# Kernel optimization log

Hardware: AMD Instinct MI355X
Metric: run time of the kernel (lower is better)

## Reference

```python
import jax, jax.numpy as jnp
import numpy as np
import math

D_MODEL, D_K, N_HEADS = 1024, 64, 16
N, T = 2, 2048


def setup_inputs() -> dict:
    key = jax.random.key(0)
    ks = jax.random.split(key, 12)
    s = 1.0 / math.sqrt(D_MODEL)
    dh = D_K * N_HEADS
    return {
        "k": jax.random.normal(ks[0], (N, T, D_MODEL), jnp.float32),
        "q": jax.random.normal(ks[1], (N, T, D_MODEL), jnp.float32),
        "v": jax.random.normal(ks[2], (N, T, D_MODEL), jnp.float32),
        "mask": jnp.ones((N, T), jnp.int32),
        "Wk": jax.random.normal(ks[3], (D_MODEL, dh), jnp.float32) * s,
        "bk": jnp.zeros((dh,), jnp.float32),
        "Wq": jax.random.normal(ks[4], (D_MODEL, dh), jnp.float32) * s,
        "bq": jnp.zeros((dh,), jnp.float32),
        "Wv": jax.random.normal(ks[5], (D_MODEL, dh), jnp.float32) * s,
        "bv": jnp.zeros((dh,), jnp.float32),
        "Wo": jax.random.normal(ks[6], (dh, D_MODEL), jnp.float32) * (1.0 / math.sqrt(dh)),
        "bo": jnp.zeros((D_MODEL,), jnp.float32),
    }


def reference(k, q, v, mask, Wk, bk, Wq, bq, Wv, bv, Wo, bo):
    n, t = k.shape[0], k.shape[1]
    # project and split heads -> (N, H, T, d_k)
    K = (k @ Wk + bk).reshape(n, t, N_HEADS, D_K).transpose(0, 2, 1, 3)
    Q = (q @ Wq + bq).reshape(n, t, N_HEADS, D_K).transpose(0, 2, 1, 3)
    V = (v @ Wv + bv).reshape(n, t, N_HEADS, D_K).transpose(0, 2, 1, 3)
    scores = jnp.einsum("bhqd,bhkd->bhqk", Q, K) / math.sqrt(D_K)
    scores = jnp.where(mask[:, None, None, :] == 0, -jnp.inf, scores)
    weights = jax.nn.softmax(scores, axis=-1)
    A = jnp.einsum("bhqk,bhkd->bhqd", weights, V)
    A = A.transpose(0, 2, 1, 3).reshape(n, t, N_HEADS * D_K)
    return A @ Wo + bo
```

## Files before the change

kernel.cpp:

```cpp
#include <hip/hip_runtime.h>


typedef __bf16 bf16;
typedef __bf16 bf16x8 __attribute__((ext_vector_type(8)));
typedef __bf16 bf16x4 __attribute__((ext_vector_type(4)));
typedef float f32x4 __attribute__((ext_vector_type(4)));

#define MFMA16(a, b, c) __builtin_amdgcn_mfma_f32_16x16x32_bf16((a), (b), (c), 0, 0, 0)

__device__ __forceinline__ void load_lds16(const bf16* g, bf16* l) {
  __builtin_amdgcn_global_load_lds(
      (const __attribute__((address_space(1))) unsigned int*)g,
      (__attribute__((address_space(3))) unsigned int*)l, 16, 0, 0);
}

__device__ __forceinline__ bf16x8 cvt8(const float* __restrict__ p) {
  const f32x4 a = *(const f32x4*)p;
  const f32x4 b = *(const f32x4*)(p + 4);
  bf16x8 r;
  r[0] = (bf16)a[0]; r[1] = (bf16)a[1]; r[2] = (bf16)a[2]; r[3] = (bf16)a[3];
  r[4] = (bf16)b[0]; r[5] = (bf16)b[1]; r[6] = (bf16)b[2]; r[7] = (bf16)b[3];
  return r;
}

__global__ __launch_bounds__(256) void convert3(const float* __restrict__ a,
                                                const float* __restrict__ b,
                                                const float* __restrict__ c,
                                                bf16* __restrict__ oa,
                                                bf16* __restrict__ ob,
                                                bf16* __restrict__ oc) {
  const size_t i = ((size_t)blockIdx.x * 256 + threadIdx.x) * 8;
  const int which = (int)(i >> 22);
  const size_t off = i & ((size_t)(1u << 22) - 1);
  const float* src = which == 0 ? a : (which == 1 ? b : c);
  bf16* dst = which == 0 ? oa : (which == 1 ? ob : oc);
  *(bf16x8*)&dst[off] = cvt8(&src[off]);
}

__global__ __launch_bounds__(256) void transposeW(
    const float* __restrict__ W0, const float* __restrict__ W1,
    const float* __restrict__ W2, const float* __restrict__ W3,
    bf16* __restrict__ T0, bf16* __restrict__ T1, bf16* __restrict__ T2,
    bf16* __restrict__ T3) {
  __shared__ bf16 t[64 * 72];
  const int z = blockIdx.z;
  const float* W = z == 0 ? W0 : (z == 1 ? W1 : (z == 2 ? W2 : W3));
  bf16* T = z == 0 ? T0 : (z == 1 ? T1 : (z == 2 ? T2 : T3));
  const int kBase = blockIdx.y * 64, nBase = blockIdx.x * 64;
  const int tid = threadIdx.x;
  const int row = tid >> 2, cs = (tid & 3) * 16;

  const float* src = &W[(size_t)(kBase + row) * 1024 + nBase + cs];
  *(bf16x8*)&t[row * 72 + cs] = cvt8(src);
  *(bf16x8*)&t[row * 72 + cs + 8] = cvt8(src + 8);
  __syncthreads();

  const int n = tid >> 2, ks = (tid & 3) * 16;
  bf16 buf[16];
#pragma unroll
  for (int j = 0; j < 16; ++j) buf[j] = t[(ks + j) * 72 + n];
  bf16* dst = &T[(size_t)(nBase + n) * 1024 + kBase + ks];
  *(bf16x8*)&dst[0] = *(bf16x8*)&buf[0];
  *(bf16x8*)&dst[8] = *(bf16x8*)&buf[8];
}

__global__ __launch_bounds__(256) void gemm_qkv(
    const bf16* __restrict__ kb, const bf16* __restrict__ vb,
    const bf16* __restrict__ qb, const bf16* __restrict__ WkT,
    const bf16* __restrict__ WvT, const bf16* __restrict__ WqT,
    const float* __restrict__ bk, const float* __restrict__ bv,
    const float* __restrict__ bq, bf16* __restrict__ K_buf,
    bf16* __restrict__ Vt_buf, bf16* __restrict__ Q_buf) {
  __shared__ __align__(16) bf16 S[12288];
  bf16* As = S;
  bf16* Ws = S + 8192;
  const int tid = threadIdx.x;
  const int lane = tid & 63, w = tid >> 6;
  const int l15 = lane & 15, quad = lane >> 4;
  const int z = blockIdx.z;
  const bf16* X = z == 0 ? kb : (z == 1 ? vb : qb);
  const bf16* WT = z == 0 ? WkT : (z == 1 ? WvT : WqT);
  const float* B = z == 0 ? bk : (z == 1 ? bv : bq);
  const int mBase = blockIdx.y * 128, nBase = blockIdx.x * 64;
  const int wm = (w >> 1) * 64, wn = (w & 1) * 32;

  const int r8 = tid >> 3;
  const int jg = ((tid & 7) ^ (r8 & 7)) * 8;
  const int sw = l15 & 7;

  f32x4 acc[4][2] = {};

  for (int k0 = 0; k0 < 1024; k0 += 64) {
    __syncthreads();
#pragma unroll
    for (int i = 0; i < 4; ++i)
      load_lds16(&X[(size_t)(mBase + r8 + i * 32) * 1024 + k0 + jg],
                 &As[(tid + i * 256) * 8]);
#pragma unroll
    for (int i = 0; i < 2; ++i)
      load_lds16(&WT[(size_t)(nBase + r8 + i * 32) * 1024 + k0 + jg],
                 &Ws[(tid + i * 256) * 8]);
    __syncthreads();

#pragma unroll
    for (int k2 = 0; k2 < 2; ++k2) {
      const int col = ((k2 * 4 + quad) ^ sw) * 8;
      bf16x8 a[4], bb[2];
#pragma unroll
      for (int mt = 0; mt < 4; ++mt)
        a[mt] = *(const bf16x8*)&As[(wm + mt * 16 + l15) * 64 + col];
#pragma unroll
      for (int nt = 0; nt < 2; ++nt)
        bb[nt] = *(const bf16x8*)&Ws[(wn + nt * 16 + l15) * 64 + col];
#pragma unroll
      for (int mt = 0; mt < 4; ++mt)
#pragma unroll
        for (int nt = 0; nt < 2; ++nt)
          acc[mt][nt] = MFMA16(a[mt], bb[nt], acc[mt][nt]);
    }
  }

  const int h = nBase >> 6;
  if (z != 1) {
    const float scale = (z == 2) ? 0.125f : 1.0f;
    bf16* o = (z == 0) ? K_buf : Q_buf;
#pragma unroll
    for (int nt = 0; nt < 2; ++nt) {
      const int n = nBase + wn + nt * 16 + l15;
      const float bias = B[n];
      const int d = n & 63;
#pragma unroll
      for (int mt = 0; mt < 4; ++mt)
#pragma unroll
        for (int r = 0; r < 4; ++r) {
          const int m = mBase + wm + mt * 16 + quad * 4 + r;
          const int b = m >> 11, t = m & 2047;
          o[((size_t)(b * 16 + h) * 2048 + t) * 64 + d] =
              (bf16)((acc[mt][nt][r] + bias) * scale);
        }
    }
  } else {
    __syncthreads();
    bf16* Tb = &S[w * 2304];
#pragma unroll
    for (int nt = 0; nt < 2; ++nt) {
      const int n = nBase + wn + nt * 16 + l15;
      const float bias = B[n];
#pragma unroll
      for (int mt = 0; mt < 4; ++mt) {
        bf16x4 pk;
#pragma unroll
        for (int r = 0; r < 4; ++r) pk[r] = (bf16)(acc[mt][nt][r] + bias);
        *(bf16x4*)&Tb[(nt * 16 + l15) * 72 + mt * 16 + quad * 4] = pk;
      }
    }
    const int b = mBase >> 11;
#pragma unroll
    for (int i = 0; i < 4; ++i) {
      const int dl = i * 8 + (lane >> 3), ts = (lane & 7) * 8;
      const bf16x8 vv = *(const bf16x8*)&Tb[dl * 72 + ts];
      const int d = wn + dl;
      const int t = (mBase + wm + ts) & 2047;
      *(bf16x8*)&Vt_buf[((size_t)(b * 16 + h) * 64 + d) * 2048 + t] = vv;
    }
  }
}

__global__ __launch_bounds__(256) void gemm_out(const bf16* __restrict__ X,
                                                const bf16* __restrict__ WT,
                                                const float* __restrict__ B,
                                                float* __restrict__ out) {
  __shared__ __align__(16) bf16 As[128 * 64];
  __shared__ __align__(16) bf16 Ws[64 * 64];
  const int tid = threadIdx.x;
  const int lane = tid & 63, w = tid >> 6;
  const int l15 = lane & 15, quad = lane >> 4;
  const int mBase = blockIdx.y * 128, nBase = blockIdx.x * 64;
  const int wm = (w >> 1) * 64, wn = (w & 1) * 32;

  const int r8 = tid >> 3;
  const int jg = ((tid & 7) ^ (r8 & 7)) * 8;
  const int sw = l15 & 7;

  f32x4 acc[4][2] = {};

  for (int k0 = 0; k0 < 1024; k0 += 64) {
    __syncthreads();
#pragma unroll
    for (int i = 0; i < 4; ++i)
      load_lds16(&X[(size_t)(mBase + r8 + i * 32) * 1024 + k0 + jg],
                 &As[(tid + i * 256) * 8]);
#pragma unroll
    for (int i = 0; i < 2; ++i)
      load_lds16(&WT[(size_t)(nBase + r8 + i * 32) * 1024 + k0 + jg],
                 &Ws[(tid + i * 256) * 8]);
    __syncthreads();

#pragma unroll
    for (int k2 = 0; k2 < 2; ++k2) {
      const int col = ((k2 * 4 + quad) ^ sw) * 8;
      bf16x8 a[4], bb[2];
#pragma unroll
      for (int mt = 0; mt < 4; ++mt)
        a[mt] = *(const bf16x8*)&As[(wm + mt * 16 + l15) * 64 + col];
#pragma unroll
      for (int nt = 0; nt < 2; ++nt)
        bb[nt] = *(const bf16x8*)&Ws[(wn + nt * 16 + l15) * 64 + col];
#pragma unroll
      for (int mt = 0; mt < 4; ++mt)
#pragma unroll
        for (int nt = 0; nt < 2; ++nt)
          acc[mt][nt] = MFMA16(a[mt], bb[nt], acc[mt][nt]);
    }
  }

#pragma unroll
  for (int nt = 0; nt < 2; ++nt) {
    const int n = nBase + wn + nt * 16 + l15;
    const float bias = B[n];
#pragma unroll
    for (int mt = 0; mt < 4; ++mt)
#pragma unroll
      for (int r = 0; r < 4; ++r) {
        const int m = mBase + wm + mt * 16 + quad * 4 + r;
        out[(size_t)m * 1024 + n] = acc[mt][nt][r] + bias;
      }
  }
}

__global__ __launch_bounds__(256) void flash_attn(const bf16* __restrict__ Q,
                                                  const bf16* __restrict__ K,
                                                  const bf16* __restrict__ Vt,
                                                  const int* __restrict__ mask,
                                                  bf16* __restrict__ A) {
  __shared__ __align__(16) bf16 Ks[64 * 64];
  __shared__ __align__(16) bf16 Vs[64 * 64];
  __shared__ __align__(16) bf16 Ps[64 * 72];
  __shared__ __align__(16) int msk[64];

  const int tid = threadIdx.x;
  const int lane = tid & 63, w = tid >> 6;
  const int l15 = lane & 15, quad = lane >> 4;
  const int bh = blockIdx.y;
  const int b = bh >> 4, h = bh & 15;
  const int qt = blockIdx.x * 64;

  const int r8 = tid >> 3;
  const int jg = ((tid & 7) ^ (r8 & 7)) * 8;
  const int sw = l15 & 7;

  const size_t qbase = ((size_t)bh * 2048 + qt + w * 16 + l15) * 64;
  const bf16x8 bq0 = *(const bf16x8*)&Q[qbase + quad * 8];
  const bf16x8 bq1 = *(const bf16x8*)&Q[qbase + 32 + quad * 8];

  f32x4 o[4] = {};
  float rs = 0.0f;

  for (int kt = 0; kt < 2048; kt += 64) {
    __syncthreads();
#pragma unroll
    for (int i = 0; i < 2; ++i) {
      const int row = r8 + i * 32;
      load_lds16(&K[((size_t)bh * 2048 + kt + row) * 64 + jg], &Ks[(tid + i * 256) * 8]);
      load_lds16(&Vt[((size_t)bh * 64 + row) * 2048 + kt + jg], &Vs[(tid + i * 256) * 8]);
    }
    if (tid < 64) msk[tid] = mask[b * 2048 + kt + tid];
    __syncthreads();

#pragma unroll
    for (int nt = 0; nt < 4; ++nt) {
      const bf16x8 ak0 = *(const bf16x8*)&Ks[(nt * 16 + l15) * 64 + ((quad ^ sw) * 8)];
      const bf16x8 ak1 = *(const bf16x8*)&Ks[(nt * 16 + l15) * 64 + (((4 + quad) ^ sw) * 8)];
      f32x4 s4 = {};
      s4 = MFMA16(ak0, bq0, s4);
      s4 = MFMA16(ak1, bq1, s4);
      const int4 mi = *(const int4*)&msk[nt * 16 + quad * 4];
      const float p0 = mi.x ? __expf(s4[0]) : 0.0f;
      const float p1 = mi.y ? __expf(s4[1]) : 0.0f;
      const float p2 = mi.z ? __expf(s4[2]) : 0.0f;
      const float p3 = mi.w ? __expf(s4[3]) : 0.0f;
      rs += (p0 + p1) + (p2 + p3);
      bf16x4 pk;
      pk[0] = (bf16)p0; pk[1] = (bf16)p1; pk[2] = (bf16)p2; pk[3] = (bf16)p3;
      *(bf16x4*)&Ps[(w * 16 + l15) * 72 + nt * 16 + quad * 4] = pk;
    }

#pragma unroll
    for (int ks = 0; ks < 2; ++ks) {
      const bf16x8 bp = *(const bf16x8*)&Ps[(w * 16 + l15) * 72 + ks * 32 + quad * 8];
#pragma unroll
      for (int mt = 0; mt < 4; ++mt) {
        const bf16x8 av =
            *(const bf16x8*)&Vs[(mt * 16 + l15) * 64 + (((ks * 4 + quad) ^ sw) * 8)];
        o[mt] = MFMA16(av, bp, o[mt]);
      }
    }
  }

  rs += __shfl_xor(rs, 16);
  rs += __shfl_xor(rs, 32);
  const float inv = rs > 0.0f ? 1.0f / rs : 0.0f;

  const int t = qt + w * 16 + l15;
  const size_t base = ((size_t)b * 2048 + t) * 1024 + h * 64;
#pragma unroll
  for (int mt = 0; mt < 4; ++mt) {
    bf16x4 ov;
#pragma unroll
    for (int r = 0; r < 4; ++r) ov[r] = (bf16)(o[mt][r] * inv);
    *(bf16x4*)&A[base + mt * 16 + quad * 4] = ov;
  }
}

extern "C" void kernel_launch(void* const* d_in, const int* in_sizes, int n_in,
                              void* d_out, int out_size, void* d_ws, size_t ws_size,
                              hipStream_t stream) {
  const float* k = (const float*)d_in[0];
  const float* q = (const float*)d_in[1];
  const float* v = (const float*)d_in[2];
  const int* mask = (const int*)d_in[3];
  const float* Wk = (const float*)d_in[4];
  const float* bk = (const float*)d_in[5];
  const float* Wq = (const float*)d_in[6];
  const float* bq = (const float*)d_in[7];
  const float* Wv = (const float*)d_in[8];
  const float* bv = (const float*)d_in[9];
  const float* Wo = (const float*)d_in[10];
  const float* bo = (const float*)d_in[11];

  const size_t ELEMS = (size_t)4 * 1024 * 1024;
  const size_t WELEMS = (size_t)1024 * 1024;

  bf16* kb = (bf16*)d_ws;
  bf16* qb = kb + ELEMS;
  bf16* vb = qb + ELEMS;
  bf16* WkT = vb + ELEMS;
  bf16* WqT = WkT + WELEMS;
  bf16* WvT = WqT + WELEMS;
  bf16* WoT = WvT + WELEMS;

  bf16* K_buf = (bf16*)d_in[0];
  bf16* Q_buf = (bf16*)d_in[0] + ELEMS;
  bf16* Vt_buf = (bf16*)d_in[2];
  bf16* A_buf = (bf16*)d_in[2] + ELEMS;

  convert3<<<6144, 256, 0, stream>>>(k, q, v, kb, qb, vb);
  transposeW<<<dim3(16, 16, 4), 256, 0, stream>>>(Wk, Wq, Wv, Wo,
                                                  WkT, WqT, WvT, WoT);
  gemm_qkv<<<dim3(16, 32, 3), 256, 0, stream>>>(kb, vb, qb, WkT, WvT, WqT,
                                                bk, bv, bq, K_buf, Vt_buf, Q_buf);
  flash_attn<<<dim3(32, 32), 256, 0, stream>>>(Q_buf, K_buf, Vt_buf, mask, A_buf);
  gemm_out<<<dim3(16, 32), 256, 0, stream>>>(A_buf, WoT, bo, (float*)d_out);
}
```

Baseline: 256.4 us.

## Double-buffer K tiles and overlap loads with MFMA using manual waitcnt

Flash attention now double-buffers the K tile in LDS and prefetches the next K tile while the current one is processed. V loads are issued early and waited on with explicit vmcnt counts, so the QK^T MFMAs and exp work run while V is still in flight. The mask is read straight from global memory into registers instead of being staged in LDS, and s_setprio raises wave priority around the MFMA sections. Relying on raw s_barrier and hand-counted vmcnt values is fragile: a wrong count, or the extra barrier being in the wrong place, could cause races on LDS.

Measured after the change: 232.8 us. 1.1x faster.

```diff
diff --git a/kernel.cpp b/kernel.cpp
--- a/kernel.cpp
+++ b/kernel.cpp
@@ -233,10 +233,9 @@
                                                   const bf16* __restrict__ Vt,
                                                   const int* __restrict__ mask,
                                                   bf16* __restrict__ A) {
-  __shared__ __align__(16) bf16 Ks[64 * 64];
+  __shared__ __align__(16) bf16 Ks[2][64 * 64];
   __shared__ __align__(16) bf16 Vs[64 * 64];
   __shared__ __align__(16) bf16 Ps[64 * 72];
-  __shared__ __align__(16) int msk[64];
 
   const int tid = threadIdx.x;
   const int lane = tid & 63, w = tid >> 6;
@@ -253,38 +252,68 @@
   const bf16x8 bq0 = *(const bf16x8*)&Q[qbase + quad * 8];
   const bf16x8 bq1 = *(const bf16x8*)&Q[qbase + 32 + quad * 8];
 
+  const int* __restrict__ mrow = &mask[b * 2048];
+
   f32x4 o[4] = {};
   float rs = 0.0f;
 
+#pragma unroll
+  for (int i = 0; i < 2; ++i)
+    load_lds16(&K[((size_t)bh * 2048 + r8 + i * 32) * 64 + jg],
+               &Ks[0][(tid + i * 256) * 8]);
+
+  int cur = 0;
   for (int kt = 0; kt < 2048; kt += 64) {
-    __syncthreads();
-#pragma unroll
-    for (int i = 0; i < 2; ++i) {
-      const int row = r8 + i * 32;
-      load_lds16(&K[((size_t)bh * 2048 + kt + row) * 64 + jg], &Ks[(tid + i * 256) * 8]);
-      load_lds16(&Vt[((size_t)bh * 64 + row) * 2048 + kt + jg], &Vs[(tid + i * 256) * 8]);
-    }
-    if (tid < 64) msk[tid] = mask[b * 2048 + kt + tid];
-    __syncthreads();
-
+    __builtin_amdgcn_s_barrier();
+
+#pragma unroll
+    for (int i = 0; i < 2; ++i)
+      load_lds16(&Vt[((size_t)bh * 64 + r8 + i * 32) * 2048 + kt + jg],
+                 &Vs[(tid + i * 256) * 8]);
+    int4 mi[4];
+#pragma unroll
+    for (int nt = 0; nt < 4; ++nt)
+      mi[nt] = *(const int4*)&mrow[kt + nt * 16 + quad * 4];
+    const int ktn = (kt + 64) & 2047;
+#pragma unroll
+    for (int i = 0; i < 2; ++i)
+      load_lds16(&K[((size_t)bh * 2048 + ktn + r8 + i * 32) * 64 + jg],
+                 &Ks[cur ^ 1][(tid + i * 256) * 8]);
+
+    asm volatile("s_waitcnt vmcnt(8)" ::: "memory");
+    __builtin_amdgcn_s_barrier();
+
+    const bf16* Kc = Ks[cur];
+    f32x4 s4[4];
+    __builtin_amdgcn_s_setprio(1);
 #pragma unroll
     for (int nt = 0; nt < 4; ++nt) {
-      const bf16x8 ak0 = *(const bf16x8*)&Ks[(nt * 16 + l15) * 64 + ((quad ^ sw) * 8)];
-      const bf16x8 ak1 = *(const bf16x8*)&Ks[(nt * 16 + l15) * 64 + (((4 + quad) ^ sw) * 8)];
-      f32x4 s4 = {};
-      s4 = MFMA16(ak0, bq0, s4);
-      s4 = MFMA16(ak1, bq1, s4);
-      const int4 mi = *(const int4*)&msk[nt * 16 + quad * 4];
-      const float p0 = mi.x ? __expf(s4[0]) : 0.0f;
-      const float p1 = mi.y ? __expf(s4[1]) : 0.0f;
-      const float p2 = mi.z ? __expf(s4[2]) : 0.0f;
-      const float p3 = mi.w ? __expf(s4[3]) : 0.0f;
+      const bf16x8 ak0 = *(const bf16x8*)&Kc[(nt * 16 + l15) * 64 + ((quad ^ sw) * 8)];
+      const bf16x8 ak1 = *(const bf16x8*)&Kc[(nt * 16 + l15) * 64 + (((4 + quad) ^ sw) * 8)];
+      f32x4 s = {};
+      s = MFMA16(ak0, bq0, s);
+      s = MFMA16(ak1, bq1, s);
+      s4[nt] = s;
+    }
+    __builtin_amdgcn_s_setprio(0);
+
+    asm volatile("s_waitcnt vmcnt(2)" ::: "memory");
+
+#pragma unroll
+    for (int nt = 0; nt < 4; ++nt) {
+      const float p0 = mi[nt].x ? __expf(s4[nt][0]) : 0.0f;
+      const float p1 = mi[nt].y ? __expf(s4[nt][1]) : 0.0f;
+      const float p2 = mi[nt].z ? __expf(s4[nt][2]) : 0.0f;
+      const float p3 = mi[nt].w ? __expf(s4[nt][3]) : 0.0f;
       rs += (p0 + p1) + (p2 + p3);
       bf16x4 pk;
       pk[0] = (bf16)p0; pk[1] = (bf16)p1; pk[2] = (bf16)p2; pk[3] = (bf16)p3;
       *(bf16x4*)&Ps[(w * 16 + l15) * 72 + nt * 16 + quad * 4] = pk;
     }
 
+    __builtin_amdgcn_s_barrier();
+
+    __builtin_amdgcn_s_setprio(1);
 #pragma unroll
     for (int ks = 0; ks < 2; ++ks) {
       const bf16x8 bp = *(const bf16x8*)&Ps[(w * 16 + l15) * 72 + ks * 32 + quad * 8];
@@ -295,6 +324,9 @@
         o[mt] = MFMA16(av, bp, o[mt]);
       }
     }
+    __builtin_amdgcn_s_setprio(0);
+
+    cur ^= 1;
   }
 
   rs += __shfl_xor(rs, 16);
```
